# Kernel optimization log

Hardware: AMD Instinct MI355X
Metric: run time of the kernel (lower is better)

The kernel has to match this reference:

```python
import jax, jax.numpy as jnp
import numpy as np


def setup_inputs() -> dict:
    key = jax.random.key(0)
    k1, k2 = jax.random.split(key)
    B, S, H, D = 2, 2048, 16, 64
    qk = jax.random.normal(k1, (B, S, 2, H, D), dtype=jnp.float32)
    v = jax.random.normal(k2, (B, S, H, D), dtype=jnp.float32)
    return {"qk": qk, "v": v}


def reference(qk, v):
    # qk: (B, S, 2, H, D); v: (B, S, H, D)
    seqlen = qk.shape[1]
    q = qk[:, :, 0]  # (B, S, H, D)
    k = qk[:, :, 1]
    # elu(x) + 1 feature map (positive features)
    q = jax.nn.elu(q) + 1.0
    k = jax.nn.elu(k) + 1.0
    # explicit O(S^2) score matrix: (B, H, T, S)
    scores = jnp.einsum('bthd,bshd->bhts', q, k)
    mask = jnp.tril(jnp.ones((seqlen, seqlen), dtype=scores.dtype))
    scores = scores * mask
    nu = scores.sum(axis=-1)  # (B, H, T)
    attention = scores / nu[:, :, :, None]
    # dropout_p = 0.0 (eval mode): identity
    output = jnp.einsum('bhts,bshd->bthd', attention, v)
    return output
```

## Files before the change

kernel.cpp:

```cpp
#include <hip/hip_runtime.h>


#define BB 2
#define SS 2048
#define HH 16
#define DD 64
#define CC 128
#define NC (SS / CC)
#define BH (BB * HH)
#define NCHUNK (BH * NC)
#define STSZ (DD * DD + DD)

#define WS_KB (512LL * 4160 * 4)
#define WS_VT (WS_KB + 512LL * 16384)
#define WS_S0 (WS_VT + 512LL * 16384)
#define WS_KZ (WS_S0 + 512LL * 8192)

typedef __attribute__((ext_vector_type(8))) short bf16x8;
typedef __attribute__((ext_vector_type(4))) short bf16x4;
typedef __attribute__((ext_vector_type(4))) float f32x4;

__device__ __forceinline__ float phi(float x) {
    return x > 0.f ? x + 1.f : __expf(x);
}
__device__ __forceinline__ unsigned short f2bf(float x) {
    unsigned int u = __float_as_uint(x);
    u += 0x7fffu + ((u >> 16) & 1u);
    return (unsigned short)(u >> 16);
}
__device__ __forceinline__ float bf2f(unsigned short b) {
    return __uint_as_float(((unsigned int)b) << 16);
}
__device__ __forceinline__ void gload16(const void* g, void* lds) {
    __builtin_amdgcn_global_load_lds(
        (const __attribute__((address_space(1))) unsigned int*)g,
        (__attribute__((address_space(3))) unsigned int*)lds, 16, 0, 0);
}

__global__ __launch_bounds__(256, 2)
void prep_state(const float* __restrict__ qk, const float* __restrict__ v,
                float* __restrict__ st, unsigned short* __restrict__ kbg,
                unsigned short* __restrict__ vtg) {
    __shared__ unsigned short Kt[DD][136];
    __shared__ unsigned short Vt[DD][136];

    const int tid = threadIdx.x, blk = blockIdx.x;
    const int bh = blk / NC, c = blk % NC, b = bh / HH, h = bh % HH;
    const int s0 = c * CC;
    const int lr = tid >> 4, lc = (tid & 15) * 4;
    char* kbc = (char*)kbg + (size_t)blk * 16384;

    #pragma unroll
    for (int it = 0; it < 8; ++it) {
        int row = it * 16 + lr;
        size_t ka = ((size_t)((b * SS + s0 + row) * 2 + 1)) * (HH * DD) + h * DD + lc;
        float4 kv = *(const float4*)(qk + ka);
        unsigned short k0 = f2bf(phi(kv.x)), k1 = f2bf(phi(kv.y));
        unsigned short k2 = f2bf(phi(kv.z)), k3 = f2bf(phi(kv.w));
        *(ushort4*)(kbc + row * 128 + ((lc * 2) ^ ((row & 7) << 4))) = make_ushort4(k0, k1, k2, k3);
        Kt[lc + 0][row] = k0; Kt[lc + 1][row] = k1;
        Kt[lc + 2][row] = k2; Kt[lc + 3][row] = k3;
        size_t va = ((size_t)((b * SS + s0 + row) * HH + h)) * DD + lc;
        float4 vv = *(const float4*)(v + va);
        Vt[lc + 0][row] = f2bf(vv.x); Vt[lc + 1][row] = f2bf(vv.y);
        Vt[lc + 2][row] = f2bf(vv.z); Vt[lc + 3][row] = f2bf(vv.w);
    }
    __syncthreads();

    {
        char* vtc = (char*)vtg + (size_t)blk * 16384;
        int e = tid >> 2, sq = (tid & 3) * 32;
        #pragma unroll
        for (int k8 = 0; k8 < 4; ++k8) {
            int s = sq + k8 * 8;
            bf16x8 val = *(const bf16x8*)&Vt[e][s];
            *(bf16x8*)(vtc + e * 256 + ((s * 2) ^ ((e & 7) << 4))) = val;
        }
    }

    const int w = tid >> 6, lane = tid & 63, g = lane >> 4, ln = lane & 15;
    bf16x8 av[4];
    #pragma unroll
    for (int ks = 0; ks < 4; ++ks)
        av[ks] = *(const bf16x8*)&Vt[w * 16 + ln][ks * 32 + g * 8];
    bf16x8 ones;
    #pragma unroll
    for (int j = 0; j < 8; ++j) ones[j] = (short)0x3F80;

    float* o = st + (size_t)blk * STSZ;
    #pragma unroll
    for (int n = 0; n < 4; ++n) {
        f32x4 a = {0.f, 0.f, 0.f, 0.f}, kz4 = {0.f, 0.f, 0.f, 0.f};
        #pragma unroll
        for (int ks = 0; ks < 4; ++ks) {
            bf16x8 bk = *(const bf16x8*)&Kt[n * 16 + ln][ks * 32 + g * 8];
            a = __builtin_amdgcn_mfma_f32_16x16x32_bf16(av[ks], bk, a, 0, 0, 0);
            kz4 = __builtin_amdgcn_mfma_f32_16x16x32_bf16(ones, bk, kz4, 0, 0, 0);
        }
        #pragma unroll
        for (int r = 0; r < 4; ++r)
            o[(w * 16 + g * 4 + r) * 64 + n * 16 + ln] = a[r];
        if (w == 0 && g == 0) o[4096 + n * 16 + ln] = kz4[0];
    }
}

__global__ __launch_bounds__(256)
void chunk_scan(const float* __restrict__ st, unsigned short* __restrict__ s0g,
                float* __restrict__ kzg) {
    int flat = blockIdx.x * 256 + threadIdx.x;
    int bh = flat / 1040, i = flat % 1040;
    if (i < 1024) {
        int i4 = i * 4;
        int e = i4 >> 6, d = i4 & 63;
        const float* src = st + (size_t)(bh * NC) * STSZ + i4;
        char* dst = (char*)s0g + (size_t)(bh * NC) * 8192
                    + e * 128 + ((d * 2) ^ ((e & 7) << 4));
        float4 run = {0.f, 0.f, 0.f, 0.f};
        #pragma unroll
        for (int c2 = 0; c2 < NC; ++c2) {
            *(ushort4*)(dst + (size_t)c2 * 8192) =
                make_ushort4(f2bf(run.x), f2bf(run.y), f2bf(run.z), f2bf(run.w));
            float4 x = *(const float4*)(src + (size_t)c2 * STSZ);
            run.x += x.x; run.y += x.y; run.z += x.z; run.w += x.w;
        }
    } else {
        int j = (i - 1024) * 4;
        const float* src = st + (size_t)(bh * NC) * STSZ + 4096 + j;
        float* dst = kzg + (size_t)(bh * NC) * 64 + j;
        float4 run = {0.f, 0.f, 0.f, 0.f};
        #pragma unroll
        for (int c2 = 0; c2 < NC; ++c2) {
            *(float4*)(dst + (size_t)c2 * 64) = run;
            float4 x = *(const float4*)(src + (size_t)c2 * STSZ);
            run.x += x.x; run.y += x.y; run.z += x.z; run.w += x.w;
        }
    }
}

__global__ __launch_bounds__(256, 3)
void lin_attn_out(const float* __restrict__ qk,
                  const unsigned short* __restrict__ kbg,
                  const unsigned short* __restrict__ vtg,
                  const unsigned short* __restrict__ s0g,
                  const float* __restrict__ kzg,
                  float* __restrict__ out) {
    __shared__ __align__(16) char KbL[16384];
    __shared__ __align__(16) char VtL[16384];
    __shared__ __align__(16) char S0L[8192];
    __shared__ float kzl[DD];
    __shared__ __align__(16) unsigned short Wl[4][16][40];
    __shared__ float nul[4][16];

    const int tid = threadIdx.x, blk = blockIdx.x;
    const int bh = blk >> 5, hc = blk & 31;
    const int c = hc >> 1, half = hc & 1;
    const int b = bh / HH, h = bh % HH;
    const int s0 = c * CC;
    const int ck = bh * NC + c;
    const int w = tid >> 6, lane = tid & 63, g = lane >> 4, ln = lane & 15;
    const int T0 = half * 64 + w * 16;

    {
        const char* kbs = (const char*)kbg + (size_t)ck * 16384;
        const char* vts = (const char*)vtg + (size_t)ck * 16384;
        const char* s0s = (const char*)s0g + (size_t)ck * 8192;
        #pragma unroll
        for (int i = 0; i < 4; ++i) {
            gload16(kbs + w * 4096 + i * 1024 + lane * 16, KbL + w * 4096 + i * 1024);
            gload16(vts + w * 4096 + i * 1024 + lane * 16, VtL + w * 4096 + i * 1024);
        }
        #pragma unroll
        for (int i = 0; i < 2; ++i)
            gload16(s0s + w * 2048 + i * 1024 + lane * 16, S0L + w * 2048 + i * 1024);
        if (tid < DD) kzl[tid] = kzg[(size_t)ck * 64 + tid];
    }

    bf16x8 aq[2];
    {
        int tg = s0 + T0 + ln;
        const float* qrow = qk + ((size_t)((b * SS + tg) * 2)) * (HH * DD) + h * DD;
        #pragma unroll
        for (int kb2 = 0; kb2 < 2; ++kb2) {
            float4 x0 = *(const float4*)(qrow + kb2 * 32 + g * 8);
            float4 x1 = *(const float4*)(qrow + kb2 * 32 + g * 8 + 4);
            bf16x8 f;
            f[0] = (short)f2bf(phi(x0.x)); f[1] = (short)f2bf(phi(x0.y));
            f[2] = (short)f2bf(phi(x0.z)); f[3] = (short)f2bf(phi(x0.w));
            f[4] = (short)f2bf(phi(x1.x)); f[5] = (short)f2bf(phi(x1.y));
            f[6] = (short)f2bf(phi(x1.z)); f[7] = (short)f2bf(phi(x1.w));
            aq[kb2] = f;
        }
    }
    __syncthreads();

    f32x4 O[4];
    #pragma unroll
    for (int n = 0; n < 4; ++n) O[n] = (f32x4){0.f, 0.f, 0.f, 0.f};

    #pragma unroll
    for (int n = 0; n < 4; ++n) {
        int e = n * 16 + ln;
        bf16x8 b0 = *(const bf16x8*)(S0L + e * 128 + ((g * 16) ^ ((e & 7) << 4)));
        bf16x8 b1 = *(const bf16x8*)(S0L + e * 128 + ((64 + g * 16) ^ ((e & 7) << 4)));
        O[n] = __builtin_amdgcn_mfma_f32_16x16x32_bf16(aq[0], b0, O[n], 0, 0, 0);
        O[n] = __builtin_amdgcn_mfma_f32_16x16x32_bf16(aq[1], b1, O[n], 0, 0, 0);
    }

    float nuA = 0.f;
    #pragma unroll
    for (int kb2 = 0; kb2 < 2; ++kb2)
        #pragma unroll
        for (int j = 0; j < 8; ++j)
            nuA = fmaf(bf2f((unsigned short)aq[kb2][j]), kzl[kb2 * 32 + g * 8 + j], nuA);

    const int dsb = T0 >> 5;
    for (int sb = 0; sb <= dsb; ++sb) {
        const bool diag = (sb == dsb);
        f32x4 Sc[2];
        #pragma unroll
        for (int ns = 0; ns < 2; ++ns) Sc[ns] = (f32x4){0.f, 0.f, 0.f, 0.f};

        #pragma unroll
        for (int ns = 0; ns < 2; ++ns) {
            int s = sb * 32 + ns * 16 + ln;
            const char* srow = KbL + s * 128;
            bf16x8 bk0 = *(const bf16x8*)(srow + ((g * 16) ^ ((s & 7) << 4)));
            bf16x8 bk1 = *(const bf16x8*)(srow + ((64 + g * 16) ^ ((s & 7) << 4)));
            Sc[ns] = __builtin_amdgcn_mfma_f32_16x16x32_bf16(aq[0], bk0, Sc[ns], 0, 0, 0);
            Sc[ns] = __builtin_amdgcn_mfma_f32_16x16x32_bf16(aq[1], bk1, Sc[ns], 0, 0, 0);
        }

        #pragma unroll
        for (int ns = 0; ns < 2; ++ns)
            #pragma unroll
            for (int r = 0; r < 4; ++r) {
                int t_cr = T0 + g * 4 + r;
                int s_cr = sb * 32 + ns * 16 + ln;
                float val = Sc[ns][r];
                if (diag && s_cr > t_cr) val = 0.f;
                Wl[w][g * 4 + r][ns * 16 + ln] = f2bf(val);
            }
        asm volatile("s_waitcnt lgkmcnt(0)" ::: "memory");
        __builtin_amdgcn_sched_barrier(0);

        bf16x8 bv[4];
        #pragma unroll
        for (int n = 0; n < 4; ++n) {
            int e = n * 16 + ln;
            bv[n] = *(const bf16x8*)(VtL + e * 256 + ((sb * 64 + g * 16) ^ ((e & 7) << 4)));
        }

        {
            const unsigned short* prow = &Wl[w][ln][0];
            bf16x4 plo = *(const bf16x4*)(prow + g * 8);
            bf16x4 phi2 = *(const bf16x4*)(prow + g * 8 + 4);
            bf16x8 pa = __builtin_shufflevector(plo, phi2, 0, 1, 2, 3, 4, 5, 6, 7);
            float rs = 0.f;
            #pragma unroll
            for (int j = 0; j < 8; ++j) rs += bf2f((unsigned short)pa[j]);
            nuA += rs;
            #pragma unroll
            for (int n = 0; n < 4; ++n)
                O[n] = __builtin_amdgcn_mfma_f32_16x16x32_bf16(pa, bv[n], O[n], 0, 0, 0);
        }
    }

    {
        float nt = nuA;
        nt += __shfl_xor(nt, 16);
        nt += __shfl_xor(nt, 32);
        if (g == 0) nul[w][ln] = nt;
    }
    asm volatile("s_waitcnt lgkmcnt(0)" ::: "memory");
    __builtin_amdgcn_sched_barrier(0);

    {
        float inv[4];
        #pragma unroll
        for (int r = 0; r < 4; ++r) inv[r] = 1.f / nul[w][g * 4 + r];
        #pragma unroll
        for (int n = 0; n < 4; ++n)
            #pragma unroll
            for (int r = 0; r < 4; ++r) {
                int t = T0 + g * 4 + r;
                int e = n * 16 + ln;
                size_t oa = ((size_t)((b * SS + s0 + t) * HH + h)) * DD + e;
                out[oa] = O[n][r] * inv[r];
            }
    }
}

extern "C" void kernel_launch(void* const* d_in, const int* in_sizes, int n_in,
                              void* d_out, int out_size, void* d_ws, size_t ws_size,
                              hipStream_t stream) {
    const float* qk = (const float*)d_in[0];
    const float* v  = (const float*)d_in[1];
    float* outp = (float*)d_out;

    float* st = (float*)d_ws;
    unsigned short* kbg = (unsigned short*)((char*)d_ws + WS_KB);
    unsigned short* vtg = (unsigned short*)((char*)d_ws + WS_VT);
    unsigned short* s0g = (unsigned short*)((char*)d_ws + WS_S0);
    float* kzg = (float*)((char*)d_ws + WS_KZ);

    prep_state<<<NCHUNK, 256, 0, stream>>>(qk, v, st, kbg, vtg);
    chunk_scan<<<130, 256, 0, stream>>>(st, s0g, kzg);
    lin_attn_out<<<NCHUNK * 2, 256, 0, stream>>>(qk, kbg, vtg, s0g, kzg, outp);
}
```

Measured before the change: 36.32 us.

## Process whole chunk per block with paired triangular tiles per wave

The output kernel now launches one block per chunk instead of two half-chunk blocks. Each wave handles two 16-row query tiles, w and 7-w, so the causal triangular work is balanced across waves, and the K/V/S0 LDS loads are shared by the whole chunk instead of being repeated per half. This halves the grid to 512 blocks and doubles register pressure per wave (two accumulator sets), which may reduce occupancy and latency hiding.

```diff
diff --git a/kernel.cpp b/kernel.cpp
--- a/kernel.cpp
+++ b/kernel.cpp
@@ -17,7 +17,6 @@
 #define WS_KZ (WS_S0 + 512LL * 8192)
 
 typedef __attribute__((ext_vector_type(8))) short bf16x8;
-typedef __attribute__((ext_vector_type(4))) short bf16x4;
 typedef __attribute__((ext_vector_type(4))) float f32x4;
 
 __device__ __forceinline__ float phi(float x) {
@@ -148,22 +147,23 @@
     __shared__ __align__(16) char VtL[16384];
     __shared__ __align__(16) char S0L[8192];
     __shared__ float kzl[DD];
-    __shared__ __align__(16) unsigned short Wl[4][16][40];
-    __shared__ float nul[4][16];
+    __shared__ __align__(16) unsigned short Wl[4][2][16][40];
+    __shared__ float nul[4][2][16];
 
     const int tid = threadIdx.x, blk = blockIdx.x;
-    const int bh = blk >> 5, hc = blk & 31;
-    const int c = hc >> 1, half = hc & 1;
-    const int b = bh / HH, h = bh % HH;
+    const int bh = blk / NC, c = blk % NC, b = bh / HH, h = bh % HH;
     const int s0 = c * CC;
-    const int ck = bh * NC + c;
     const int w = tid >> 6, lane = tid & 63, g = lane >> 4, ln = lane & 15;
-    const int T0 = half * 64 + w * 16;
+
+    const int tA = w;
+    const int tB = 7 - w;
+    const int nA = (w >> 1) + 1;
+    const int nB = (9 - w) >> 1;
 
     {
-        const char* kbs = (const char*)kbg + (size_t)ck * 16384;
-        const char* vts = (const char*)vtg + (size_t)ck * 16384;
-        const char* s0s = (const char*)s0g + (size_t)ck * 8192;
+        const char* kbs = (const char*)kbg + (size_t)blk * 16384;
+        const char* vts = (const char*)vtg + (size_t)blk * 16384;
+        const char* s0s = (const char*)s0g + (size_t)blk * 8192;
         #pragma unroll
         for (int i = 0; i < 4; ++i) {
             gload16(kbs + w * 4096 + i * 1024 + lane * 16, KbL + w * 4096 + i * 1024);
@@ -172,73 +172,103 @@
         #pragma unroll
         for (int i = 0; i < 2; ++i)
             gload16(s0s + w * 2048 + i * 1024 + lane * 16, S0L + w * 2048 + i * 1024);
-        if (tid < DD) kzl[tid] = kzg[(size_t)ck * 64 + tid];
-    }
-
-    bf16x8 aq[2];
-    {
-        int tg = s0 + T0 + ln;
-        const float* qrow = qk + ((size_t)((b * SS + tg) * 2)) * (HH * DD) + h * DD;
-        #pragma unroll
-        for (int kb2 = 0; kb2 < 2; ++kb2) {
-            float4 x0 = *(const float4*)(qrow + kb2 * 32 + g * 8);
-            float4 x1 = *(const float4*)(qrow + kb2 * 32 + g * 8 + 4);
-            bf16x8 f;
-            f[0] = (short)f2bf(phi(x0.x)); f[1] = (short)f2bf(phi(x0.y));
-            f[2] = (short)f2bf(phi(x0.z)); f[3] = (short)f2bf(phi(x0.w));
-            f[4] = (short)f2bf(phi(x1.x)); f[5] = (short)f2bf(phi(x1.y));
-            f[6] = (short)f2bf(phi(x1.z)); f[7] = (short)f2bf(phi(x1.w));
-            aq[kb2] = f;
-        }
+        if (tid < DD) kzl[tid] = kzg[(size_t)blk * 64 + tid];
+    }
+
+    bf16x8 aqA[2], aqB[2];
+    #pragma unroll
+    for (int kb2 = 0; kb2 < 2; ++kb2) {
+        const float* qrowA = qk + ((size_t)((b * SS + s0 + tA * 16 + ln) * 2)) * (HH * DD) + h * DD;
+        const float* qrowB = qk + ((size_t)((b * SS + s0 + tB * 16 + ln) * 2)) * (HH * DD) + h * DD;
+        float4 a0 = *(const float4*)(qrowA + kb2 * 32 + g * 8);
+        float4 a1 = *(const float4*)(qrowA + kb2 * 32 + g * 8 + 4);
+        float4 b0 = *(const float4*)(qrowB + kb2 * 32 + g * 8);
+        float4 b1 = *(const float4*)(qrowB + kb2 * 32 + g * 8 + 4);
+        bf16x8 fa, fb;
+        fa[0] = (short)f2bf(phi(a0.x)); fa[1] = (short)f2bf(phi(a0.y));
+        fa[2] = (short)f2bf(phi(a0.z)); fa[3] = (short)f2bf(phi(a0.w));
+        fa[4] = (short)f2bf(phi(a1.x)); fa[5] = (short)f2bf(phi(a1.y));
+        fa[6] = (short)f2bf(phi(a1.z)); fa[7] = (short)f2bf(phi(a1.w));
+        fb[0] = (short)f2bf(phi(b0.x)); fb[1] = (short)f2bf(phi(b0.y));
+        fb[2] = (short)f2bf(phi(b0.z)); fb[3] = (short)f2bf(phi(b0.w));
+        fb[4] = (short)f2bf(phi(b1.x)); fb[5] = (short)f2bf(phi(b1.y));
+        fb[6] = (short)f2bf(phi(b1.z)); fb[7] = (short)f2bf(phi(b1.w));
+        aqA[kb2] = fa;
+        aqB[kb2] = fb;
     }
     __syncthreads();
 
-    f32x4 O[4];
-    #pragma unroll
-    for (int n = 0; n < 4; ++n) O[n] = (f32x4){0.f, 0.f, 0.f, 0.f};
+    f32x4 OA[4], OB[4];
+    #pragma unroll
+    for (int n = 0; n < 4; ++n) {
+        OA[n] = (f32x4){0.f, 0.f, 0.f, 0.f};
+        OB[n] = (f32x4){0.f, 0.f, 0.f, 0.f};
+    }
 
     #pragma unroll
     for (int n = 0; n < 4; ++n) {
         int e = n * 16 + ln;
-        bf16x8 b0 = *(const bf16x8*)(S0L + e * 128 + ((g * 16) ^ ((e & 7) << 4)));
-        bf16x8 b1 = *(const bf16x8*)(S0L + e * 128 + ((64 + g * 16) ^ ((e & 7) << 4)));
-        O[n] = __builtin_amdgcn_mfma_f32_16x16x32_bf16(aq[0], b0, O[n], 0, 0, 0);
-        O[n] = __builtin_amdgcn_mfma_f32_16x16x32_bf16(aq[1], b1, O[n], 0, 0, 0);
-    }
-
-    float nuA = 0.f;
+        bf16x8 s0b0 = *(const bf16x8*)(S0L + e * 128 + ((g * 16) ^ ((e & 7) << 4)));
+        bf16x8 s0b1 = *(const bf16x8*)(S0L + e * 128 + ((64 + g * 16) ^ ((e & 7) << 4)));
+        OA[n] = __builtin_amdgcn_mfma_f32_16x16x32_bf16(aqA[0], s0b0, OA[n], 0, 0, 0);
+        OA[n] = __builtin_amdgcn_mfma_f32_16x16x32_bf16(aqA[1], s0b1, OA[n], 0, 0, 0);
+        OB[n] = __builtin_amdgcn_mfma_f32_16x16x32_bf16(aqB[0], s0b0, OB[n], 0, 0, 0);
+        OB[n] = __builtin_amdgcn_mfma_f32_16x16x32_bf16(aqB[1], s0b1, OB[n], 0, 0, 0);
+    }
+
+    float nuA = 0.f, nuB = 0.f;
     #pragma unroll
     for (int kb2 = 0; kb2 < 2; ++kb2)
         #pragma unroll
-        for (int j = 0; j < 8; ++j)
-            nuA = fmaf(bf2f((unsigned short)aq[kb2][j]), kzl[kb2 * 32 + g * 8 + j], nuA);
-
-    const int dsb = T0 >> 5;
-    for (int sb = 0; sb <= dsb; ++sb) {
-        const bool diag = (sb == dsb);
-        f32x4 Sc[2];
-        #pragma unroll
-        for (int ns = 0; ns < 2; ++ns) Sc[ns] = (f32x4){0.f, 0.f, 0.f, 0.f};
-
+        for (int j = 0; j < 8; ++j) {
+            float kzv = kzl[kb2 * 32 + g * 8 + j];
+            nuA = fmaf(bf2f((unsigned short)aqA[kb2][j]), kzv, nuA);
+            nuB = fmaf(bf2f((unsigned short)aqB[kb2][j]), kzv, nuB);
+        }
+
+    for (int sb = 0; sb < nB; ++sb) {
+        const bool doA = (sb < nA);
+        const bool diagA = (sb == nA - 1);
+        const bool diagB = (sb == nB - 1);
+
+        bf16x8 bk[2][2];
         #pragma unroll
         for (int ns = 0; ns < 2; ++ns) {
             int s = sb * 32 + ns * 16 + ln;
             const char* srow = KbL + s * 128;
-            bf16x8 bk0 = *(const bf16x8*)(srow + ((g * 16) ^ ((s & 7) << 4)));
-            bf16x8 bk1 = *(const bf16x8*)(srow + ((64 + g * 16) ^ ((s & 7) << 4)));
-            Sc[ns] = __builtin_amdgcn_mfma_f32_16x16x32_bf16(aq[0], bk0, Sc[ns], 0, 0, 0);
-            Sc[ns] = __builtin_amdgcn_mfma_f32_16x16x32_bf16(aq[1], bk1, Sc[ns], 0, 0, 0);
+            bk[ns][0] = *(const bf16x8*)(srow + ((g * 16) ^ ((s & 7) << 4)));
+            bk[ns][1] = *(const bf16x8*)(srow + ((64 + g * 16) ^ ((s & 7) << 4)));
+        }
+
+        f32x4 ScA[2], ScB[2];
+        #pragma unroll
+        for (int ns = 0; ns < 2; ++ns) {
+            ScB[ns] = (f32x4){0.f, 0.f, 0.f, 0.f};
+            ScB[ns] = __builtin_amdgcn_mfma_f32_16x16x32_bf16(aqB[0], bk[ns][0], ScB[ns], 0, 0, 0);
+            ScB[ns] = __builtin_amdgcn_mfma_f32_16x16x32_bf16(aqB[1], bk[ns][1], ScB[ns], 0, 0, 0);
+        }
+        if (doA) {
+            #pragma unroll
+            for (int ns = 0; ns < 2; ++ns) {
+                ScA[ns] = (f32x4){0.f, 0.f, 0.f, 0.f};
+                ScA[ns] = __builtin_amdgcn_mfma_f32_16x16x32_bf16(aqA[0], bk[ns][0], ScA[ns], 0, 0, 0);
+                ScA[ns] = __builtin_amdgcn_mfma_f32_16x16x32_bf16(aqA[1], bk[ns][1], ScA[ns], 0, 0, 0);
+            }
         }
 
         #pragma unroll
         for (int ns = 0; ns < 2; ++ns)
             #pragma unroll
             for (int r = 0; r < 4; ++r) {
-                int t_cr = T0 + g * 4 + r;
-                int s_cr = sb * 32 + ns * 16 + ln;
-                float val = Sc[ns][r];
-                if (diag && s_cr > t_cr) val = 0.f;
-                Wl[w][g * 4 + r][ns * 16 + ln] = f2bf(val);
+                int s_glob = sb * 32 + ns * 16 + ln;
+                float vb = ScB[ns][r];
+                if (diagB && s_glob > tB * 16 + g * 4 + r) vb = 0.f;
+                Wl[w][1][g * 4 + r][ns * 16 + ln] = f2bf(vb);
+                if (doA) {
+                    float va = ScA[ns][r];
+                    if (diagA && s_glob > tA * 16 + g * 4 + r) va = 0.f;
+                    Wl[w][0][g * 4 + r][ns * 16 + ln] = f2bf(va);
+                }
             }
         asm volatile("s_waitcnt lgkmcnt(0)" ::: "memory");
         __builtin_amdgcn_sched_barrier(0);
@@ -251,38 +281,51 @@
         }
 
         {
-            const unsigned short* prow = &Wl[w][ln][0];
-            bf16x4 plo = *(const bf16x4*)(prow + g * 8);
-            bf16x4 phi2 = *(const bf16x4*)(prow + g * 8 + 4);
-            bf16x8 pa = __builtin_shufflevector(plo, phi2, 0, 1, 2, 3, 4, 5, 6, 7);
+            bf16x8 pb = *(const bf16x8*)&Wl[w][1][ln][g * 8];
+            float rs = 0.f;
+            #pragma unroll
+            for (int j = 0; j < 8; ++j) rs += bf2f((unsigned short)pb[j]);
+            nuB += rs;
+            #pragma unroll
+            for (int n = 0; n < 4; ++n)
+                OB[n] = __builtin_amdgcn_mfma_f32_16x16x32_bf16(pb, bv[n], OB[n], 0, 0, 0);
+        }
+        if (doA) {
+            bf16x8 pa = *(const bf16x8*)&Wl[w][0][ln][g * 8];
             float rs = 0.f;
             #pragma unroll
             for (int j = 0; j < 8; ++j) rs += bf2f((unsigned short)pa[j]);
             nuA += rs;
             #pragma unroll
             for (int n = 0; n < 4; ++n)
-                O[n] = __builtin_amdgcn_mfma_f32_16x16x32_bf16(pa, bv[n], O[n], 0, 0, 0);
+                OA[n] = __builtin_amdgcn_mfma_f32_16x16x32_bf16(pa, bv[n], OA[n], 0, 0, 0);
         }
     }
 
     {
-        float nt = nuA;
-        nt += __shfl_xor(nt, 16);
-        nt += __shfl_xor(nt, 32);
-        if (g == 0) nul[w][ln] = nt;
+        float na = nuA, nb = nuB;
+        na += __shfl_xor(na, 16); na += __shfl_xor(na, 32);
+        nb += __shfl_xor(nb, 16); nb += __shfl_xor(nb, 32);
+        if (g == 0) {
+            nul[w][0][ln] = na;
+            nul[w][1][ln] = nb;
+        }
     }
     asm volatile("s_waitcnt lgkmcnt(0)" ::: "memory");
     __builtin_amdgcn_sched_barrier(0);
 
-    {
+    #pragma unroll
+    for (int tile = 0; tile < 2; ++tile) {
+        const f32x4* O = tile ? OB : OA;
+        int tbase = (tile ? tB : tA) * 16;
         float inv[4];
         #pragma unroll
-        for (int r = 0; r < 4; ++r) inv[r] = 1.f / nul[w][g * 4 + r];
+        for (int r = 0; r < 4; ++r) inv[r] = 1.f / nul[w][tile][g * 4 + r];
         #pragma unroll
         for (int n = 0; n < 4; ++n)
             #pragma unroll
             for (int r = 0; r < 4; ++r) {
-                int t = T0 + g * 4 + r;
+                int t = tbase + g * 4 + r;
                 int e = n * 16 + ln;
                 size_t oa = ((size_t)((b * SS + s0 + t) * HH + h)) * DD + e;
                 out[oa] = O[n][r] * inv[r];
@@ -305,5 +348,5 @@
 
     prep_state<<<NCHUNK, 256, 0, stream>>>(qk, v, st, kbg, vtg);
     chunk_scan<<<130, 256, 0, stream>>>(st, s0g, kzg);
-    lin_attn_out<<<NCHUNK * 2, 256, 0, stream>>>(qk, kbg, vtg, s0g, kzg, outp);
-}
+    lin_attn_out<<<NCHUNK, 256, 0, stream>>>(qk, kbg, vtg, s0g, kzg, outp);
+}
```

After: 33.78 us. 1.08x faster.
